# Performance work log

Hardware: AMD Instinct MI355X
Metric: run time of the kernel (lower is better)

Reference implementation:

```python
import jax, jax.numpy as jnp
import numpy as np


def _apply_rope(q, k):
    # q, k: [BH, T, hd]
    hd = q.shape[-1]
    half = hd // 2
    T = q.shape[1]
    inv_freq = 1.0 / (10000.0 ** (jnp.arange(half, dtype=jnp.float32) / half))
    freqs = jnp.arange(T, dtype=jnp.float32)[:, None] * inv_freq[None, :]  # [T, half]
    cos = jnp.cos(freqs)[None, :, :]
    sin = jnp.sin(freqs)[None, :, :]
    q1, q2 = q[..., :half], q[..., half:]
    k1, k2 = k[..., :half], k[..., half:]
    q_rot = jnp.concatenate([q1 * cos - q2 * sin, q1 * sin + q2 * cos], axis=-1)
    k_rot = jnp.concatenate([k1 * cos - k2 * sin, k1 * sin + k2 * cos], axis=-1)
    return q_rot, k_rot


def setup_inputs() -> dict:
    key = jax.random.key(0)
    ks = jax.random.split(key, 5)
    B, T, D = 2, 2048, 1024
    x = jax.random.normal(ks[0], (B, T, D), dtype=jnp.float32)
    w_qkv = jax.random.normal(ks[1], (D, 3 * D), dtype=jnp.float32) * (1.0 / np.sqrt(D))
    b_qkv = jax.random.normal(ks[2], (3 * D,), dtype=jnp.float32) * 0.01
    w_out = jax.random.normal(ks[3], (D, D), dtype=jnp.float32) * (1.0 / np.sqrt(D))
    b_out = jax.random.normal(ks[4], (D,), dtype=jnp.float32) * 0.01
    return {"x": x, "w_qkv": w_qkv, "b_qkv": b_qkv, "w_out": w_out, "b_out": b_out}


def reference(x, w_qkv, b_qkv, w_out, b_out):
    B, T, D = x.shape
    H = 16
    hd = D // H
    qkv = x @ w_qkv + b_qkv  # [B, T, 3D]
    q, k, v = jnp.split(qkv, 3, axis=-1)
    # [B, T, H, hd] -> [B, H, T, hd]
    q = q.reshape(B, T, H, hd).transpose(0, 2, 1, 3)
    k = k.reshape(B, T, H, hd).transpose(0, 2, 1, 3)
    v = v.reshape(B, T, H, hd).transpose(0, 2, 1, 3)
    q, k = _apply_rope(q.reshape(B * H, T, hd), k.reshape(B * H, T, hd))
    q = q.reshape(B, H, T, hd)
    k = k.reshape(B, H, T, hd)
    scores = jnp.einsum("bhqd,bhkd->bhqk", q, k) / jnp.sqrt(jnp.float32(hd))
    attn = jax.nn.softmax(scores, axis=-1)
    out = jnp.einsum("bhqk,bhkd->bhqd", attn, v)  # [B, H, T, hd]
    out = out.transpose(0, 2, 1, 3).reshape(B, T, D)
    return out @ w_out + b_out
```

## Files before the change

### kernel.cpp

```cpp
#include <hip/hip_runtime.h>
#include <hip/hip_bf16.h>
#include <stdint.h>


typedef __bf16 bf16;
typedef __bf16 bf16x8 __attribute__((ext_vector_type(8)));
typedef __bf16 bf16x4 __attribute__((ext_vector_type(4)));
typedef float  f32x4  __attribute__((ext_vector_type(4)));

__device__ __forceinline__ void gload16(void* lds, const void* g) {
  __builtin_amdgcn_global_load_lds((__attribute__((address_space(1))) void*)(void*)g,
                                   (__attribute__((address_space(3))) void*)lds, 16, 0, 0);
}


__global__ void k_convert_x(const float* __restrict__ x, bf16* __restrict__ xb, int n) {
  int i = (blockIdx.x * blockDim.x + threadIdx.x) * 4;
  if (i >= n) return;
  float4 v = *(const float4*)(x + i);
  bf16x4 o;
  o.x = (bf16)v.x; o.y = (bf16)v.y; o.z = (bf16)v.z; o.w = (bf16)v.w;
  *(bf16x4*)(xb + i) = o;
}

__global__ void k_transpose_bf16(const float* __restrict__ in, bf16* __restrict__ out,
                                 int rows, int cols) {
  __shared__ float t[32][33];
  int c0 = blockIdx.x * 32, r0 = blockIdx.y * 32;
  for (int i = threadIdx.y; i < 32; i += 8)
    t[i][threadIdx.x] = in[(size_t)(r0 + i) * cols + c0 + threadIdx.x];
  __syncthreads();
  for (int i = threadIdx.y; i < 32; i += 8)
    out[(size_t)(c0 + i) * rows + r0 + threadIdx.x] = (bf16)t[threadIdx.x][i];
}


__global__ __launch_bounds__(256)
void k_gemm_qkv(const bf16* __restrict__ A, const bf16* __restrict__ Bt,
                const float* __restrict__ bias, bf16* __restrict__ Qd,
                bf16* __restrict__ Kd, bf16* __restrict__ Vtd) {
  alignas(16) __shared__ bf16 lds_a[128 * 32];
  alignas(16) __shared__ bf16 lds_b[128 * 32];
  const int tid = threadIdx.x;
  const int lane = tid & 63, w = tid >> 6;
  const int wr = w >> 1, wc = w & 1;
  const int bid = blockIdx.x;
  const int swz = (bid & 7) * 96 + (bid >> 3);
  const int br = swz / 24, bc = swz % 24;
  const int r16 = lane & 15, g4 = lane >> 4;

  f32x4 acc[4][4] = {};
  const bf16* gA = A + (size_t)(br * 128 + (lane >> 2)) * 1024 + (lane & 3) * 8;
  const bf16* gB = Bt + (size_t)(bc * 128 + (lane >> 2)) * 1024 + (lane & 3) * 8;

  for (int kt = 0; kt < 32; ++kt) {
    const int ko = kt * 32;
#pragma unroll
    for (int it = 0; it < 2; ++it) {
      const int row0 = 16 * (4 * it + w);
      gload16(&lds_a[row0 * 32], gA + (size_t)row0 * 1024 + ko);
      gload16(&lds_b[row0 * 32], gB + (size_t)row0 * 1024 + ko);
    }
    __syncthreads();
    bf16x8 af[4], bfr[4];
#pragma unroll
    for (int m = 0; m < 4; ++m)
      af[m] = *(const bf16x8*)&lds_a[(wr * 64 + 16 * m + r16) * 32 + g4 * 8];
#pragma unroll
    for (int n = 0; n < 4; ++n)
      bfr[n] = *(const bf16x8*)&lds_b[(wc * 64 + 16 * n + r16) * 32 + g4 * 8];
#pragma unroll
    for (int m = 0; m < 4; ++m)
#pragma unroll
      for (int n = 0; n < 4; ++n)
        acc[m][n] = __builtin_amdgcn_mfma_f32_16x16x32_bf16(af[m], bfr[n], acc[m][n], 0, 0, 0);
    __syncthreads();
  }

  const int reg = bc >> 3;
  const int h = ((bc & 7) << 1) | wc;
  const float bq = 0.125f * 1.4426950408889634f;
  const float Lc = 13.287712379549449f / 32.0f;
  const float inv2pi = 0.15915494309189535f;
  const float if0r = exp2f(-(float)r16 * Lc) * inv2pi;
  const float if1r = exp2f(-(float)(16 + r16) * Lc) * inv2pi;
  float bv[4];
#pragma unroll
  for (int n = 0; n < 4; ++n) bv[n] = bias[bc * 128 + wc * 64 + 16 * n + r16];

  if (reg == 2) {
#pragma unroll
    for (int m = 0; m < 4; ++m) {
      const int row0 = br * 128 + wr * 64 + 16 * m + 4 * g4;
      const int t0 = row0 & 2047, b = row0 >> 11;
      const int pos = (t0 & ~63) | (((t0 >> 2) & 3) << 4) | (((t0 >> 5) & 1) << 3) |
                      (((t0 >> 4) & 1) << 2);
#pragma unroll
      for (int n = 0; n < 4; ++n) {
        bf16x4 pk;
#pragma unroll
        for (int r = 0; r < 4; ++r) pk[r] = (bf16)(acc[m][n][r] + bv[n]);
        *(bf16x4*)(Vtd + ((size_t)((b * 16 + h) * 64) + 16 * n + r16) * 2048 + pos) = pk;
      }
    }
  } else {
    bf16* dst = (reg == 0) ? Qd : Kd;
#pragma unroll
    for (int m = 0; m < 4; ++m) {
#pragma unroll
      for (int r = 0; r < 4; ++r) {
        const int row = br * 128 + wr * 64 + 16 * m + 4 * g4 + r;
        const int t = row & 2047, b = row >> 11;
        bf16* o = dst + ((size_t)(b * 16 + h) * 2048 + t) * 64;
        const float v0 = acc[m][0][r] + bv[0];
        const float v1 = acc[m][1][r] + bv[1];
        const float v2 = acc[m][2][r] + bv[2];
        const float v3 = acc[m][3][r] + bv[3];
        const float tf = (float)t;
        float rv0 = tf * if0r; rv0 -= floorf(rv0);
        float rv1 = tf * if1r; rv1 -= floorf(rv1);
        const float s0 = __builtin_amdgcn_sinf(rv0), c0 = __builtin_amdgcn_cosf(rv0);
        const float s1 = __builtin_amdgcn_sinf(rv1), c1 = __builtin_amdgcn_cosf(rv1);
        float r0 = v0 * c0 - v2 * s0, r2 = v0 * s0 + v2 * c0;
        float r1 = v1 * c1 - v3 * s1, r3 = v1 * s1 + v3 * c1;
        if (reg == 0) { r0 *= bq; r1 *= bq; r2 *= bq; r3 *= bq; }
        o[r16]      = (bf16)r0;
        o[16 + r16] = (bf16)r1;
        o[32 + r16] = (bf16)r2;
        o[48 + r16] = (bf16)r3;
      }
    }
  }
}


__global__ __launch_bounds__(256)
void k_gemm_out(const bf16* __restrict__ A, const bf16* __restrict__ Bt,
                const float* __restrict__ bias, float* __restrict__ Cp,
                int M, int N, int K) {
  alignas(16) __shared__ bf16 lds_a[64 * 32];
  alignas(16) __shared__ bf16 lds_b[128 * 32];
  const int tid = threadIdx.x;
  const int lane = tid & 63, w = tid >> 6;
  const int nb = N >> 7;
  const int nwg = gridDim.x;
  const int bid = blockIdx.x;
  const int swz = (bid & 7) * (nwg >> 3) + (bid >> 3);
  const int br = swz / nb, bc = swz % nb;
  const int r16 = lane & 15, g4 = lane >> 4;

  f32x4 acc[4][2] = {};
  const int nk = K >> 5;
  const bf16* gA = A + (size_t)(br * 64 + 16 * w + (lane >> 2)) * K + (lane & 3) * 8;
  const bf16* gB = Bt + (size_t)(bc * 128 + (lane >> 2)) * K + (lane & 3) * 8;

  for (int kt = 0; kt < nk; ++kt) {
    const int ko = kt * 32;
    gload16(&lds_a[w * 512], gA + ko);
#pragma unroll
    for (int c = 0; c < 2; ++c) {
      const int row0 = 16 * (2 * w + c);
      gload16(&lds_b[row0 * 32], gB + (size_t)row0 * K + ko);
    }
    __syncthreads();
    bf16x8 af[4], bfr[2];
#pragma unroll
    for (int m = 0; m < 4; ++m)
      af[m] = *(const bf16x8*)&lds_a[(16 * m + r16) * 32 + g4 * 8];
#pragma unroll
    for (int n = 0; n < 2; ++n)
      bfr[n] = *(const bf16x8*)&lds_b[(32 * w + 16 * n + r16) * 32 + g4 * 8];
#pragma unroll
    for (int m = 0; m < 4; ++m)
#pragma unroll
      for (int n = 0; n < 2; ++n)
        acc[m][n] = __builtin_amdgcn_mfma_f32_16x16x32_bf16(af[m], bfr[n], acc[m][n], 0, 0, 0);
    __syncthreads();
  }

#pragma unroll
  for (int m = 0; m < 4; ++m) {
    const int row = br * 64 + 16 * m + 4 * g4;
#pragma unroll
    for (int n = 0; n < 2; ++n) {
      const int col = bc * 128 + 32 * w + 16 * n + r16;
      const float bvv = bias[col];
#pragma unroll
      for (int r = 0; r < 4; ++r)
        Cp[(size_t)(row + r) * N + col] = acc[m][n][r] + bvv;
    }
  }
}


__global__ __launch_bounds__(512)
void k_attn(const bf16* __restrict__ Qg, const bf16* __restrict__ Kg,
            const bf16* __restrict__ Vtg, bf16* __restrict__ PO,
            float* __restrict__ lsum) {
  alignas(16) __shared__ char smem[33280];
  bf16* kbufs = (bf16*)smem;
  bf16* vbufs = (bf16*)(smem + 16384);
  const int tid = threadIdx.x, lane = tid & 63, w = tid >> 6;
  const int bid = blockIdx.x;
  const int swz = (bid & 7) * 128 + (bid >> 3);
  const int half = swz & 1;
  const int id2 = swz >> 1;
  const int bh = id2 >> 4, q0 = (id2 & 15) * 128;
  const int qh = w >> 1, kh = w & 1;
  const int r16 = lane & 15, g4 = lane >> 4;
  const char* Kb  = (const char*)(Kg  + (size_t)bh * 2048 * 64);
  const char* Vtb = (const char*)(Vtg + (size_t)bh * 64 * 2048);
  const bf16* Qb  = Qg + (size_t)bh * 2048 * 64;

  const int rl = lane >> 3;
  const int colx = ((lane & 7) * 16) ^ (rl << 4);

  bf16x8 qf[2][2];
#pragma unroll
  for (int g = 0; g < 2; ++g) {
    const int qrow = q0 + 32 * qh + 16 * g + r16;
    qf[g][0] = *(const bf16x8*)(Qb + (size_t)qrow * 64 + g4 * 8);
    qf[g][1] = *(const bf16x8*)(Qb + (size_t)qrow * 64 + 32 + g4 * 8);
  }

  f32x4 O[2][4] = {};
  f32x4 O4[2] = {};
  bf16x8 ones8 = {};
  if (r16 == 0)
#pragma unroll
    for (int j = 0; j < 8; ++j) ones8[j] = (bf16)1.f;

#define STAGE(bufi, t0)                                                          \
  {                                                                              \
    const int row = 8 * w + rl;                                                  \
    gload16(&kbufs[(bufi) * 4096 + w * 512],                                     \
            Kb + (size_t)((t0) + row) * 128 + colx);                             \
    gload16(&vbufs[(bufi) * 4096 + w * 512],                                     \
            Vtb + (size_t)row * 4096 + (size_t)(t0) * 2 + colx);                 \
  }

  const int it0 = half * 16;
  STAGE(0, it0 * 64);
  __syncthreads();

  const int rsw = (r16 & 7) << 4;

#pragma unroll 1
  for (int ii = 0; ii < 16; ++ii) {
    const int bsel = ii & 1;
    if (ii + 1 < 16) STAGE(bsel ^ 1, (it0 + ii + 1) * 64);
    const char* kb = (const char*)kbufs + bsel * 8192 + r16 * 128;
    const char* vb = (const char*)vbufs + bsel * 8192 + r16 * 128;

    f32x4 S[2][2];
#pragma unroll
    for (int nl = 0; nl < 2; ++nl) {
      const int n = 2 * kh + nl;
      bf16x8 kf0 = *(const bf16x8*)(kb + n * 2048 + ((g4 * 16) ^ rsw));
      bf16x8 kf1 = *(const bf16x8*)(kb + n * 2048 + ((64 + g4 * 16) ^ rsw));
      f32x4 s = {};
      s = __builtin_amdgcn_mfma_f32_16x16x32_bf16(kf0, qf[0][0], s, 0, 0, 0);
      s = __builtin_amdgcn_mfma_f32_16x16x32_bf16(kf1, qf[0][1], s, 0, 0, 0);
      S[0][nl] = s;
      f32x4 t = {};
      t = __builtin_amdgcn_mfma_f32_16x16x32_bf16(kf0, qf[1][0], t, 0, 0, 0);
      t = __builtin_amdgcn_mfma_f32_16x16x32_bf16(kf1, qf[1][1], t, 0, 0, 0);
      S[1][nl] = t;
    }

    bf16x8 pb[2];
#pragma unroll
    for (int g = 0; g < 2; ++g)
#pragma unroll
      for (int nl = 0; nl < 2; ++nl)
#pragma unroll
        for (int r = 0; r < 4; ++r)
          pb[g][nl * 4 + r] = (bf16)exp2f(S[g][nl][r]);

#pragma unroll
    for (int dn = 0; dn < 4; ++dn) {
      bf16x8 vf = *(const bf16x8*)(vb + dn * 2048 + ((32 * g4 + 16 * kh) ^ rsw));
      O[0][dn] = __builtin_amdgcn_mfma_f32_16x16x32_bf16(vf, pb[0], O[0][dn], 0, 0, 0);
      O[1][dn] = __builtin_amdgcn_mfma_f32_16x16x32_bf16(vf, pb[1], O[1][dn], 0, 0, 0);
    }
    O4[0] = __builtin_amdgcn_mfma_f32_16x16x32_bf16(ones8, pb[0], O4[0], 0, 0, 0);
    O4[1] = __builtin_amdgcn_mfma_f32_16x16x32_bf16(ones8, pb[1], O4[1], 0, 0, 0);
    __syncthreads();
  }
#undef STAGE

  float* obuf = (float*)smem;
  float* lbuf = (float*)(smem + 32768);
  if (kh == 1) {
#pragma unroll
    for (int g = 0; g < 2; ++g) {
#pragma unroll
      for (int dn = 0; dn < 4; ++dn)
        *(f32x4*)&obuf[(qh * 32 + g * 16 + r16) * 64 + 16 * dn + 4 * g4] = O[g][dn];
      if (g4 == 0) lbuf[qh * 32 + g * 16 + r16] = O4[g][0];
    }
  }
  __syncthreads();
  if (kh == 0) {
    bf16* POh = PO + (size_t)half * 4194304;
#pragma unroll
    for (int g = 0; g < 2; ++g) {
      const int row = bh * 2048 + q0 + 32 * qh + 16 * g + r16;
      const float ls = __shfl(O4[g][0], r16, 64) + lbuf[qh * 32 + g * 16 + r16];
#pragma unroll
      for (int dn = 0; dn < 4; ++dn) {
        f32x4 os = O[g][dn];
        f32x4 ot = *(const f32x4*)&obuf[(qh * 32 + g * 16 + r16) * 64 + 16 * dn + 4 * g4];
        bf16x4 ov;
#pragma unroll
        for (int r = 0; r < 4; ++r) ov[r] = (bf16)(os[r] + ot[r]);
        *(bf16x4*)(POh + (size_t)row * 64 + 16 * dn + 4 * g4) = ov;
      }
      if (g4 == 0) lsum[half * 65536 + row] = ls;
    }
  }
}


__global__ __launch_bounds__(256)
void k_combine(const bf16* __restrict__ PO, const float* __restrict__ lsum,
               bf16* __restrict__ attnb) {
  const int idx = blockIdx.x * 256 + threadIdx.x;
  const int row = idx >> 3, seg = idx & 7;
  const float inv = 1.f / (lsum[row] + lsum[65536 + row]);
  bf16x8 p0 = *(const bf16x8*)(PO + (size_t)row * 64 + seg * 8);
  bf16x8 p1 = *(const bf16x8*)(PO + 4194304 + (size_t)row * 64 + seg * 8);
  bf16x8 o;
#pragma unroll
  for (int j = 0; j < 8; ++j)
    o[j] = (bf16)(((float)p0[j] + (float)p1[j]) * inv);
  const int bh = row >> 11, t = row & 2047;
  const int b = bh >> 4, h = bh & 15;
  *(bf16x8*)(attnb + ((size_t)(b * 2048 + t)) * 1024 + h * 64 + seg * 8) = o;
}


extern "C" void kernel_launch(void* const* d_in, const int* in_sizes, int n_in,
                              void* d_out, int out_size, void* d_ws, size_t ws_size,
                              hipStream_t stream) {
  const float* x     = (const float*)d_in[0];
  const float* w_qkv = (const float*)d_in[1];
  const float* b_qkv = (const float*)d_in[2];
  const float* w_out = (const float*)d_in[3];
  const float* b_out = (const float*)d_in[4];
  float* out = (float*)d_out;

  char* ws = (char*)d_ws;
  bf16* xb    = (bf16*)(ws);
  bf16* wqkvT = (bf16*)(ws + 8388608);
  bf16* Qb    = (bf16*)(ws + 16777216);
  bf16* Kb    = (bf16*)(ws + 25165824);
  bf16* Vtb   = (bf16*)(ws + 33554432);
  bf16* attnb = (bf16*)(ws + 41943040);
  bf16* woutT = (bf16*)(ws + 50331648);
  float* lsum = (float*)(ws + 52428800);
  bf16* PO    = (bf16*)(ws);

  k_convert_x<<<4096 * 1024 / 4 / 256, 256, 0, stream>>>(x, xb, 4096 * 1024);
  k_transpose_bf16<<<dim3(3072 / 32, 1024 / 32), dim3(32, 8), 0, stream>>>(w_qkv, wqkvT, 1024, 3072);
  k_transpose_bf16<<<dim3(1024 / 32, 1024 / 32), dim3(32, 8), 0, stream>>>(w_out, woutT, 1024, 1024);
  k_gemm_qkv<<<32 * 24, 256, 0, stream>>>(xb, wqkvT, b_qkv, Qb, Kb, Vtb);
  k_attn<<<1024, 512, 0, stream>>>(Qb, Kb, Vtb, PO, lsum);
  k_combine<<<2048, 256, 0, stream>>>(PO, lsum, attnb);
  k_gemm_out<<<512, 256, 0, stream>>>(attnb, woutT, b_out, out, 4096, 1024, 1024);
}
```

Before: 129.5 us.

## Halve QKV GEMM tile rows and remap waves so each lane does one RoPE pair

The QKV projection GEMM tile shrinks from 128x128 to 64x128, doubling the grid to 1536 workgroups. Each wave now covers all 64 rows and two 16-column blocks paired so a lane holds matching first-half and second-half RoPE dimensions, so it needs one sin/cos pair per row instead of two. The aim is better CU occupancy and load balance, since the old 768-block grid was small, and a lighter epilogue. The cost is lower arithmetic intensity per tile and more redundant loads of the B operand.

```diff
diff --git a/kernel.cpp b/kernel.cpp
--- a/kernel.cpp
+++ b/kernel.cpp
@@ -39,69 +39,68 @@
 void k_gemm_qkv(const bf16* __restrict__ A, const bf16* __restrict__ Bt,
                 const float* __restrict__ bias, bf16* __restrict__ Qd,
                 bf16* __restrict__ Kd, bf16* __restrict__ Vtd) {
-  alignas(16) __shared__ bf16 lds_a[128 * 32];
+  alignas(16) __shared__ bf16 lds_a[64 * 32];
   alignas(16) __shared__ bf16 lds_b[128 * 32];
   const int tid = threadIdx.x;
   const int lane = tid & 63, w = tid >> 6;
-  const int wr = w >> 1, wc = w & 1;
   const int bid = blockIdx.x;
-  const int swz = (bid & 7) * 96 + (bid >> 3);
+  const int swz = (bid & 7) * 192 + (bid >> 3);
   const int br = swz / 24, bc = swz % 24;
   const int r16 = lane & 15, g4 = lane >> 4;
 
-  f32x4 acc[4][4] = {};
-  const bf16* gA = A + (size_t)(br * 128 + (lane >> 2)) * 1024 + (lane & 3) * 8;
+  f32x4 acc[4][2] = {};
+  const bf16* gA = A + (size_t)(br * 64 + 16 * w + (lane >> 2)) * 1024 + (lane & 3) * 8;
   const bf16* gB = Bt + (size_t)(bc * 128 + (lane >> 2)) * 1024 + (lane & 3) * 8;
 
   for (int kt = 0; kt < 32; ++kt) {
     const int ko = kt * 32;
-#pragma unroll
-    for (int it = 0; it < 2; ++it) {
-      const int row0 = 16 * (4 * it + w);
-      gload16(&lds_a[row0 * 32], gA + (size_t)row0 * 1024 + ko);
+    gload16(&lds_a[w * 512], gA + ko);
+#pragma unroll
+    for (int c = 0; c < 2; ++c) {
+      const int row0 = 16 * (2 * w + c);
       gload16(&lds_b[row0 * 32], gB + (size_t)row0 * 1024 + ko);
     }
     __syncthreads();
-    bf16x8 af[4], bfr[4];
+    bf16x8 af[4], bfr[2];
 #pragma unroll
     for (int m = 0; m < 4; ++m)
-      af[m] = *(const bf16x8*)&lds_a[(wr * 64 + 16 * m + r16) * 32 + g4 * 8];
-#pragma unroll
-    for (int n = 0; n < 4; ++n)
-      bfr[n] = *(const bf16x8*)&lds_b[(wc * 64 + 16 * n + r16) * 32 + g4 * 8];
+      af[m] = *(const bf16x8*)&lds_a[(16 * m + r16) * 32 + g4 * 8];
+#pragma unroll
+    for (int n = 0; n < 2; ++n)
+      bfr[n] = *(const bf16x8*)&lds_b[((w >> 1) * 64 + (w & 1) * 16 + 32 * n + r16) * 32 + g4 * 8];
 #pragma unroll
     for (int m = 0; m < 4; ++m)
 #pragma unroll
-      for (int n = 0; n < 4; ++n)
+      for (int n = 0; n < 2; ++n)
         acc[m][n] = __builtin_amdgcn_mfma_f32_16x16x32_bf16(af[m], bfr[n], acc[m][n], 0, 0, 0);
     __syncthreads();
   }
 
   const int reg = bc >> 3;
-  const int h = ((bc & 7) << 1) | wc;
+  const int h = ((bc & 7) << 1) | (w >> 1);
+  const int i = 16 * (w & 1) + r16;
   const float bq = 0.125f * 1.4426950408889634f;
   const float Lc = 13.287712379549449f / 32.0f;
   const float inv2pi = 0.15915494309189535f;
-  const float if0r = exp2f(-(float)r16 * Lc) * inv2pi;
-  const float if1r = exp2f(-(float)(16 + r16) * Lc) * inv2pi;
-  float bv[4];
-#pragma unroll
-  for (int n = 0; n < 4; ++n) bv[n] = bias[bc * 128 + wc * 64 + 16 * n + r16];
+  const float ifr = exp2f(-(float)i * Lc) * inv2pi;
+  const float bv0 = bias[bc * 128 + (w >> 1) * 64 + i];
+  const float bv2 = bias[bc * 128 + (w >> 1) * 64 + 32 + i];
 
   if (reg == 2) {
 #pragma unroll
     for (int m = 0; m < 4; ++m) {
-      const int row0 = br * 128 + wr * 64 + 16 * m + 4 * g4;
+      const int row0 = br * 64 + 16 * m + 4 * g4;
       const int t0 = row0 & 2047, b = row0 >> 11;
       const int pos = (t0 & ~63) | (((t0 >> 2) & 3) << 4) | (((t0 >> 5) & 1) << 3) |
                       (((t0 >> 4) & 1) << 2);
-#pragma unroll
-      for (int n = 0; n < 4; ++n) {
-        bf16x4 pk;
-#pragma unroll
-        for (int r = 0; r < 4; ++r) pk[r] = (bf16)(acc[m][n][r] + bv[n]);
-        *(bf16x4*)(Vtd + ((size_t)((b * 16 + h) * 64) + 16 * n + r16) * 2048 + pos) = pk;
+      bf16x4 pk0, pk2;
+#pragma unroll
+      for (int r = 0; r < 4; ++r) {
+        pk0[r] = (bf16)(acc[m][0][r] + bv0);
+        pk2[r] = (bf16)(acc[m][1][r] + bv2);
       }
+      *(bf16x4*)(Vtd + ((size_t)((b * 16 + h) * 64) + i) * 2048 + pos) = pk0;
+      *(bf16x4*)(Vtd + ((size_t)((b * 16 + h) * 64) + 32 + i) * 2048 + pos) = pk2;
     }
   } else {
     bf16* dst = (reg == 0) ? Qd : Kd;
@@ -109,25 +108,17 @@
     for (int m = 0; m < 4; ++m) {
 #pragma unroll
       for (int r = 0; r < 4; ++r) {
-        const int row = br * 128 + wr * 64 + 16 * m + 4 * g4 + r;
+        const int row = br * 64 + 16 * m + 4 * g4 + r;
         const int t = row & 2047, b = row >> 11;
         bf16* o = dst + ((size_t)(b * 16 + h) * 2048 + t) * 64;
-        const float v0 = acc[m][0][r] + bv[0];
-        const float v1 = acc[m][1][r] + bv[1];
-        const float v2 = acc[m][2][r] + bv[2];
-        const float v3 = acc[m][3][r] + bv[3];
-        const float tf = (float)t;
-        float rv0 = tf * if0r; rv0 -= floorf(rv0);
-        float rv1 = tf * if1r; rv1 -= floorf(rv1);
-        const float s0 = __builtin_amdgcn_sinf(rv0), c0 = __builtin_amdgcn_cosf(rv0);
-        const float s1 = __builtin_amdgcn_sinf(rv1), c1 = __builtin_amdgcn_cosf(rv1);
-        float r0 = v0 * c0 - v2 * s0, r2 = v0 * s0 + v2 * c0;
-        float r1 = v1 * c1 - v3 * s1, r3 = v1 * s1 + v3 * c1;
-        if (reg == 0) { r0 *= bq; r1 *= bq; r2 *= bq; r3 *= bq; }
-        o[r16]      = (bf16)r0;
-        o[16 + r16] = (bf16)r1;
-        o[32 + r16] = (bf16)r2;
-        o[48 + r16] = (bf16)r3;
+        const float v0 = acc[m][0][r] + bv0;
+        const float v2 = acc[m][1][r] + bv2;
+        float rv = (float)t * ifr; rv -= floorf(rv);
+        const float s = __builtin_amdgcn_sinf(rv), c = __builtin_amdgcn_cosf(rv);
+        float r0 = v0 * c - v2 * s, r2 = v0 * s + v2 * c;
+        if (reg == 0) { r0 *= bq; r2 *= bq; }
+        o[i]      = (bf16)r0;
+        o[32 + i] = (bf16)r2;
       }
     }
   }
@@ -364,7 +355,7 @@
   k_convert_x<<<4096 * 1024 / 4 / 256, 256, 0, stream>>>(x, xb, 4096 * 1024);
   k_transpose_bf16<<<dim3(3072 / 32, 1024 / 32), dim3(32, 8), 0, stream>>>(w_qkv, wqkvT, 1024, 3072);
   k_transpose_bf16<<<dim3(1024 / 32, 1024 / 32), dim3(32, 8), 0, stream>>>(w_out, woutT, 1024, 1024);
-  k_gemm_qkv<<<32 * 24, 256, 0, stream>>>(xb, wqkvT, b_qkv, Qb, Kb, Vtb);
+  k_gemm_qkv<<<1536, 256, 0, stream>>>(xb, wqkvT, b_qkv, Qb, Kb, Vtb);
   k_attn<<<1024, 512, 0, stream>>>(Qb, Kb, Vtb, PO, lsum);
   k_combine<<<2048, 256, 0, stream>>>(PO, lsum, attnb);
   k_gemm_out<<<512, 256, 0, stream>>>(attnb, woutT, b_out, out, 4096, 1024, 1024);
```

New measurement: 146.9 us. 13.5% more time.
